# Kernel tuning notes

Hardware: AMD Instinct MI355X
Metric: run time of the kernel (lower is better)

The kernel has to match this reference:

```python
import jax, jax.numpy as jnp
import numpy as np

B, S, D, H = 32, 512, 512, 8
DF = D // H  # dim_feature = 64
NEG_INF = -1e32


def setup_inputs() -> dict:
    key = jax.random.key(0)
    ks = jax.random.split(key, 8)
    std = 1.0 / np.sqrt(D)  # xavier-ish scale for square linears
    return {
        "q": jax.random.normal(ks[0], (B, S, D), jnp.float32),
        "k": jax.random.normal(ks[1], (B, S, D), jnp.float32),
        "v": jax.random.normal(ks[2], (B, S, D), jnp.float32),
        "mask": jnp.tril(jnp.ones((S, S), jnp.int32))[None, None],  # causal AKT mask
        "zero_pad": 1,
        "question_difficulty_emb": jax.random.normal(ks[3], (B, S, S), jnp.float32) * 0.1,
        "Wk": jax.random.normal(ks[4], (D, D), jnp.float32) * std,
        "bk": jnp.zeros((D,), jnp.float32),
        "Wv": jax.random.normal(ks[5], (D, D), jnp.float32) * std,
        "bv": jnp.zeros((D,), jnp.float32),
        "Wo": jax.random.normal(ks[6], (D, D), jnp.float32) * std,
        "bo": jnp.zeros((D,), jnp.float32),
        "gammas": jax.random.normal(ks[7], (H, 1, 1), jnp.float32) * 0.1,
    }


def reference(q, k, v, mask, zero_pad, question_difficulty_emb, Wk, bk, Wv, bv, Wo, bo, gammas):
    bs = q.shape[0]

    def proj(x, W, b):
        # Linear then split heads: [B,S,D] -> [B,H,S,DF]
        return (x @ W.T + b).reshape(bs, -1, H, DF).transpose(0, 2, 1, 3)

    qh = proj(q, Wk, bk)  # key_query_same=True: q uses key_linear
    kh = proj(k, Wk, bk)
    vh = proj(v, Wv, bv)

    scores = jnp.einsum("bhqd,bhkd->bhqk", qh, kh) / jnp.sqrt(jnp.float32(DF))
    seqlen = scores.shape[-1]
    maskb = mask == 0  # [1,1,S,S]

    # --- distance-decay term (computed under no_grad in torch, detached) ---
    scores_ = jax.nn.softmax(jnp.where(maskb, NEG_INF, scores), axis=-1)
    scores_ = scores_ * mask.astype(scores.dtype)
    distcum = jnp.cumsum(scores_, axis=-1)                      # [B,H,S,S]
    disttot = jnp.sum(scores_, axis=-1, keepdims=True)          # [B,H,S,1]
    pos = jnp.abs(jnp.arange(seqlen)[None, :] - jnp.arange(seqlen)[:, None]).astype(scores.dtype)
    dist_scores = jnp.sqrt(jnp.clip((disttot - distcum) * pos[None, None], 0.0))
    dist_scores = jax.lax.stop_gradient(dist_scores)

    gamma = -jax.nn.softplus(gammas)[None]                      # [1,H,1,1]
    diff = jnp.exp(jax.nn.sigmoid(question_difficulty_emb))[:, None]  # [B,1,S,S]
    total_effect = jnp.clip(jnp.exp(dist_scores * gamma * diff), 1e-5, 1e5)

    scores = scores * total_effect
    scores = jax.nn.softmax(jnp.where(maskb, NEG_INF, scores), axis=-1)
    if zero_pad:
        scores = scores.at[:, :, 0, :].set(0.0)  # zero first query row
    scores = jnp.where(maskb, 0.0, scores)
    # dropout p=0 (eval) -> identity

    out = jnp.einsum("bhqk,bhkd->bhqd", scores, vh)
    concat = out.transpose(0, 2, 1, 3).reshape(bs, -1, D)
    return concat @ Wo.T + bo
```

## Files before the change

### kernel.cpp

```cpp
#include <hip/hip_runtime.h>

typedef unsigned short u16;
typedef __attribute__((ext_vector_type(8))) short short8;
typedef __attribute__((ext_vector_type(8))) _Float16 h8;
typedef __attribute__((ext_vector_type(4))) float f32x4;

__device__ __forceinline__ float b2f(u16 u) {
    return __uint_as_float(((unsigned int)u) << 16);
}
__device__ __forceinline__ u16 f2b(float f) {
    unsigned int x = __float_as_uint(f);
    return (u16)((x + 0x7FFFu + ((x >> 16) & 1u)) >> 16);
}
__device__ __forceinline__ float ldf(const void* p, size_t i, bool f32) {
    return f32 ? ((const float*)p)[i] : b2f(((const u16*)p)[i]);
}
__device__ __forceinline__ void stf(void* p, size_t i, bool f32, float v) {
    if (f32) ((float*)p)[i] = v; else ((u16*)p)[i] = f2b(v);
}
__device__ __forceinline__ float ex2(float x) {
    float r; asm("v_exp_f32 %0, %1" : "=v"(r) : "v"(x)); return r;
}

__device__ __forceinline__ void ldsld16(const void* g, void* l) {
    __builtin_amdgcn_global_load_lds(
        (const __attribute__((address_space(1))) unsigned int*)g,
        (__attribute__((address_space(3))) unsigned int*)l, 16, 0, 0);
}

__global__ void detect_f32(const u16* __restrict__ q, int* __restrict__ flag) {
    __shared__ int cw, cz;
    if (threadIdx.x == 0) { cw = 0; cz = 0; }
    __syncthreads();
    int w = 0, z = 0;
    for (int i = threadIdx.x; i < 4096; i += 256) {
        u16 u = q[i];
        int e = (u >> 7) & 0xFF;
        if (e >= 0xC8) w++;
        if (((i & 1) == 0) && u == 0) z++;
    }
    atomicAdd(&cw, w); atomicAdd(&cz, z);
    __syncthreads();
    if (threadIdx.x == 0) *flag = (cw > 8 || cz > 1024) ? 1 : 0;
}

__global__ __launch_bounds__(256) void cvt3(
    const void* __restrict__ s0, const void* __restrict__ s1,
    const void* __restrict__ s2, u16* __restrict__ d0, u16* __restrict__ d1,
    u16* __restrict__ d2, int n, const int* __restrict__ flag)
{
    const bool f32 = (*flag) != 0;
    const int z = blockIdx.z;
    const void* src = (z == 0) ? s0 : (z == 1) ? s1 : s2;
    u16* dst = (z == 0) ? d0 : (z == 1) ? d1 : d2;
    const int i = (blockIdx.x * 256 + threadIdx.x) * 8;
    if (i >= n) return;
    short8 o;
    if (f32) {
        const float4* s = (const float4*)((const float*)src + i);
        float4 v0 = s[0], v1 = s[1];
        o[0] = (short)f2b(v0.x); o[1] = (short)f2b(v0.y);
        o[2] = (short)f2b(v0.z); o[3] = (short)f2b(v0.w);
        o[4] = (short)f2b(v1.x); o[5] = (short)f2b(v1.y);
        o[6] = (short)f2b(v1.z); o[7] = (short)f2b(v1.w);
    } else {
        o = *(const short8*)((const u16*)src + i);
    }
    *(short8*)(dst + i) = o;
}

__global__ __launch_bounds__(256) void prep_diff(
    const void* __restrict__ qde, _Float16* __restrict__ diff, int n,
    const int* __restrict__ flag)
{
    const bool f32 = (*flag) != 0;
    const int i = (blockIdx.x * 256 + threadIdx.x) * 8;
    if (i >= n) return;
    float x[8];
    if (f32) {
        const float4* s = (const float4*)((const float*)qde + i);
        float4 v0 = s[0], v1 = s[1];
        x[0] = v0.x; x[1] = v0.y; x[2] = v0.z; x[3] = v0.w;
        x[4] = v1.x; x[5] = v1.y; x[6] = v1.z; x[7] = v1.w;
    } else {
        short8 v8 = *(const short8*)((const u16*)qde + i);
        #pragma unroll
        for (int j = 0; j < 8; ++j) x[j] = b2f((u16)v8[j]);
    }
    h8 o;
    #pragma unroll
    for (int j = 0; j < 8; ++j) {
        float sig = __builtin_amdgcn_rcpf(1.f + __expf(-x[j]));
        o[j] = (_Float16)__expf(sig);
    }
    *(h8*)(diff + i) = o;
}

#define BM 128
#define BN 128
#define BK 32

__device__ __forceinline__ void gemm_body(
    const u16* __restrict__ A, const u16* __restrict__ W,
    const void* __restrict__ bias, void* __restrict__ dst,
    bool f32, int mode, int bm, int bn, int M, int N, int K)
{
    __shared__ u16 As[BM * BK];
    __shared__ u16 Bs[BN * BK];
    const int t = threadIdx.x;
    const int w = t >> 6, l = t & 63, lq = l & 15, quad = l >> 4;
    const int wr = (w >> 1) * 64, wc = (w & 1) * 64;

    const int whalf = (w & 1) * 64;
    const u16* gsrc = (w < 2) ? A : W;
    const int  gbase = (w < 2) ? bm : bn;
    u16* lbase = (w < 2) ? As : Bs;

    f32x4 acc[4][4] = {};

    for (int k0 = 0; k0 < K; k0 += BK) {
        __syncthreads();
        #pragma unroll
        for (int c = 0; c < 4; ++c) {
            const int row = whalf + c * 16 + (l >> 2);
            ldsld16(gsrc + (size_t)(gbase + row) * K + k0 + (l & 3) * 8,
                    lbase + row * BK + (l & 3) * 8);
        }
        asm volatile("s_waitcnt vmcnt(0)" ::: "memory");
        __syncthreads();
        short8 af[4], bf[4];
        #pragma unroll
        for (int i = 0; i < 4; ++i)
            af[i] = *(const short8*)&As[(wr + i * 16 + lq) * BK + quad * 8];
        #pragma unroll
        for (int j = 0; j < 4; ++j)
            bf[j] = *(const short8*)&Bs[(wc + j * 16 + lq) * BK + quad * 8];
        #pragma unroll
        for (int i = 0; i < 4; ++i)
            #pragma unroll
            for (int j = 0; j < 4; ++j)
                acc[i][j] = __builtin_amdgcn_mfma_f32_16x16x32_bf16(
                    af[i], bf[j], acc[i][j], 0, 0, 0);
    }

    #pragma unroll
    for (int j = 0; j < 4; ++j) {
        const int n = bn + wc + j * 16 + lq;
        const float bb = ldf(bias, n, f32);
        #pragma unroll
        for (int i = 0; i < 4; ++i) {
            #pragma unroll
            for (int r = 0; r < 4; ++r) {
                const int m = bm + wr + i * 16 + quad * 4 + r;
                const float vout = acc[i][j][r] + bb;
                if (mode == 0) {
                    const int b = m >> 9, s = m & 511, hh = n >> 6, df = n & 63;
                    ((u16*)dst)[((((size_t)b * 8 + hh) * 512 + s) << 6) + df] = f2b(vout);
                } else if (mode == 2) {
                    const int b = m >> 9, s = m & 511, hh = n >> 6, df = n & 63;
                    ((u16*)dst)[((((size_t)b * 8 + hh) * 64 + df) << 9) + s] = f2b(vout);
                } else {
                    stf(dst, (size_t)m * N + n, f32, vout);
                }
            }
        }
    }
}

__global__ __launch_bounds__(256) void proj3(
    const u16* __restrict__ cq, const u16* __restrict__ ck,
    const u16* __restrict__ cv, const u16* __restrict__ cWk,
    const u16* __restrict__ cWv, const void* __restrict__ bk,
    const void* __restrict__ bv, u16* __restrict__ qh, u16* __restrict__ kh,
    u16* __restrict__ vt, const int* __restrict__ flag, int M, int N, int K)
{
    const int z = blockIdx.z;
    const u16* A = (z == 0) ? cq : (z == 1) ? ck : cv;
    const u16* W = (z < 2) ? cWk : cWv;
    const void* bias = (z < 2) ? bk : bv;
    void* dst = (z == 0) ? (void*)qh : (z == 1) ? (void*)kh : (void*)vt;
    gemm_body(A, W, bias, dst, (*flag) != 0, (z < 2) ? 0 : 2,
              blockIdx.y * BM, blockIdx.x * BN, M, N, K);
}

__global__ __launch_bounds__(256) void gemm_out(
    const u16* __restrict__ A, const u16* __restrict__ W,
    const void* __restrict__ bias, void* __restrict__ dst,
    const int* __restrict__ flag, int M, int N, int K)
{
    gemm_body(A, W, bias, dst, (*flag) != 0, 1,
              blockIdx.y * BM, blockIdx.x * BN, M, N, K);
}

#define QT  16
#define SRS 568
#define PRS 584

__global__ __launch_bounds__(512) void akt_attn(
    const u16* __restrict__ qh, const u16* __restrict__ kh,
    const u16* __restrict__ vt, const _Float16* __restrict__ diff,
    const void* __restrict__ gammas, const int* __restrict__ zero_pad,
    const int* __restrict__ flag, u16* __restrict__ attn)
{
    __shared__ _Float16 s_h[QT * SRS];
    __shared__ u16      p_lds[QT * PRS];

    const int blk = blockIdx.x;
    const int h = blk & 7;
    const int i0 = blk >> 3;
    const int qt = i0 & 31;
    const int b = i0 >> 5;

    const int q0 = qt * QT;
    const int t = threadIdx.x, w = t >> 6, l = t & 63;
    const int lq = l & 15, quad = l >> 4;
    const bool f32 = (*flag) != 0;
    const size_t bh = ((size_t)b * 8 + h) * 512;
    const int qmax = q0 + QT - 1;

    {
        const u16* qb = qh + (bh + q0) * 64;
        short8 af0 = *(const short8*)(qb + lq * 64 +      quad * 8);
        short8 af1 = *(const short8*)(qb + lq * 64 + 32 + quad * 8);
        const u16* kb = kh + bh * 64;
        const int KT = (q0 + QT + 127) >> 7;
        int n0 = w * 16;
        bool act = (n0 <= qmax);
        short8 bf0, bf1;
        if (act) {
            bf0 = *(const short8*)(kb + (size_t)(n0 + lq) * 64 +      quad * 8);
            bf1 = *(const short8*)(kb + (size_t)(n0 + lq) * 64 + 32 + quad * 8);
        }
        for (int kt = 0; kt < KT; ++kt) {
            const int n0n = (kt + 1) * 128 + w * 16;
            const bool actn = (kt + 1 < KT) && (n0n <= qmax);
            short8 nb0, nb1;
            if (actn) {
                nb0 = *(const short8*)(kb + (size_t)(n0n + lq) * 64 +      quad * 8);
                nb1 = *(const short8*)(kb + (size_t)(n0n + lq) * 64 + 32 + quad * 8);
            }
            if (act) {
                f32x4 acc = {0.f, 0.f, 0.f, 0.f};
                acc = __builtin_amdgcn_mfma_f32_16x16x32_bf16(af0, bf0, acc, 0, 0, 0);
                acc = __builtin_amdgcn_mfma_f32_16x16x32_bf16(af1, bf1, acc, 0, 0, 0);
                const int cm = n0 + lq + 8 * (n0 >> 6);
                #pragma unroll
                for (int r = 0; r < 4; ++r)
                    s_h[(quad * 4 + r) * SRS + cm] =
                        (_Float16)(acc[r] * 0.180336880f);
            }
            bf0 = nb0; bf1 = nb1; act = actn; n0 = n0n;
        }
    }
    __syncthreads();

    {
        const float g = ldf(gammas, h, f32);
        const float gl2 = -log1pf(expf(g)) * 1.4426950408889634f;
        const int zp = zero_pad[0];
        const int c0 = l * 8;
        #pragma unroll
        for (int rr = 0; rr < 2; ++rr) {
            const int row = w * 2 + rr;
            const int q = q0 + row;
            const size_t qoff = ((size_t)b * 512 + q) * 512 + c0;
            h8 dv = *(const h8*)(diff + qoff);
            h8 sv16 = *(const h8*)(s_h + row * SRS + c0 + 8 * (l >> 3));
            float sv[8], cs[8];
            float run = 0.f;
            #pragma unroll
            for (int j = 0; j < 8; ++j) {
                float s = (c0 + j <= q) ? (float)sv16[j] : -1e30f;
                sv[j] = s;
                float p = ex2(s);
                run += p; cs[j] = run;
            }
            float incl = run;
            #pragma unroll
            for (int o = 1; o < 64; o <<= 1) {
                float u = __shfl_up(incl, o, 64);
                if (l >= o) incl += u;
            }
            const float ls   = __shfl(incl, 63, 64);
            const float inv1 = __builtin_amdgcn_rcpf(ls);
            const float t0   = ls - incl + run;
            const float qf   = (float)(q - c0);
            float f8[8]; float lf = 0.f;
            #pragma unroll
            for (int j = 0; j < 8; ++j) {
                float suf  = t0 - cs[j];
                float pos  = qf - (float)j;
                float m    = fmaxf(suf * pos, 0.f) * inv1;
                float dist = __builtin_amdgcn_sqrtf(m);
                float a    = fmaxf(dist * gl2 * (float)dv[j], -16.609640474f);
                float eff  = ex2(a);
                float f    = ex2(sv[j] * eff);
                f8[j] = f; lf += f;
            }
            #pragma unroll
            for (int o = 32; o > 0; o >>= 1) lf += __shfl_xor(lf, o, 64);
            float inv2 = __builtin_amdgcn_rcpf(lf);
            if (zp && q == 0) inv2 = 0.f;
            short8 pb;
            #pragma unroll
            for (int j = 0; j < 8; ++j) pb[j] = (short)f2b(f8[j] * inv2);
            *(short8*)(p_lds + row * PRS + c0 + 8 * (l >> 3)) = pb;
        }
    }
    __syncthreads();

    {
        const int g = w & 3;
        const int half = w >> 2;
        const int KS = (qmax >> 5) + 1;
        const u16* vb = vt + ((size_t)(b * 8 + h) * 64 + g * 16 + lq) * 512;
        const u16* prow = p_lds + lq * PRS;
        f32x4 oacc = {0.f, 0.f, 0.f, 0.f};
        for (int ks = half; ks < KS; ks += 2) {
            const int kb2 = ks * 32 + quad * 8;
            short8 pa = *(const short8*)(prow + kb2 + 8 * (kb2 >> 6));
            short8 vv = *(const short8*)(vb + kb2);
            oacc = __builtin_amdgcn_mfma_f32_16x16x32_bf16(pa, vv, oacc, 0, 0, 0);
        }
        float* opart = (float*)s_h;
        if (half == 1) {
            #pragma unroll
            for (int r = 0; r < 4; ++r)
                opart[(g * 16 + quad * 4 + r) * 17 + lq] = oacc[r];
        }
        __syncthreads();
        if (half == 0) {
            const size_t ob = ((size_t)b * 512 + q0 + quad * 4) * 512 + h * 64 + g * 16 + lq;
            #pragma unroll
            for (int r = 0; r < 4; ++r)
                attn[ob + (size_t)r * 512] =
                    f2b(oacc[r] + opart[(g * 16 + quad * 4 + r) * 17 + lq]);
        }
    }
}

extern "C" void kernel_launch(void* const* d_in, const int* in_sizes, int n_in,
                              void* d_out, int out_size, void* d_ws, size_t ws_size,
                              hipStream_t stream) {
    const void* q   = d_in[0];
    const void* k   = d_in[1];
    const void* v   = d_in[2];
    const int*  zp  = (const int*)d_in[4];
    const void* qde = d_in[5];
    const void* Wk  = d_in[6];
    const void* bk  = d_in[7];
    const void* Wv  = d_in[8];
    const void* bv  = d_in[9];
    const void* Wo  = d_in[10];
    const void* bo  = d_in[11];
    const void* gam = d_in[12];

    const int M = 32 * 512, N = 512, K = 512;
    const int NBIG = M * K;
    const int NW = 512 * 512;

    char* ws = (char*)d_ws;
    int* flag = (int*)ws;
    const size_t SZB = (size_t)NBIG * 2;
    const size_t SZW = (size_t)NW * 2;
    u16* cWk  = (u16*)(ws + 1024);
    u16* cWv  = (u16*)(ws + 1024 + SZW);
    u16* cWo  = (u16*)(ws + 1024 + 2 * SZW);
    u16* cq   = (u16*)(ws + 1024 + 3 * SZW);
    u16* ck   = (u16*)(ws + 1024 + 3 * SZW + SZB);
    u16* cv   = (u16*)(ws + 1024 + 3 * SZW + 2 * SZB);
    u16* qh   = (u16*)(ws + 1024 + 3 * SZW + 3 * SZB);
    u16* kh   = (u16*)(ws + 1024 + 3 * SZW + 4 * SZB);
    u16* vt   = (u16*)(ws + 1024 + 3 * SZW + 5 * SZB);
    u16* attn = (u16*)(ws + 1024 + 3 * SZW + 6 * SZB);

    detect_f32<<<1, 256, 0, stream>>>((const u16*)q, flag);
    cvt3<<<dim3(NW / 2048, 1, 3), 256, 0, stream>>>(Wk, Wv, Wo, cWk, cWv, cWo, NW, flag);
    cvt3<<<dim3(NBIG / 2048, 1, 3), 256, 0, stream>>>(q, k, v, cq, ck, cv, NBIG, flag);
    proj3<<<dim3(N / BN, M / BM, 3), 256, 0, stream>>>(
        cq, ck, cv, cWk, cWv, bk, bv, qh, kh, vt, flag, M, N, K);
    _Float16* diffb = (_Float16*)cq;
    prep_diff<<<dim3(NBIG / 2048), 256, 0, stream>>>(qde, diffb, NBIG, flag);
    akt_attn<<<8192, 512, 0, stream>>>(qh, kh, vt, diffb, gam, zp, flag, attn);
    gemm_out<<<dim3(N / BN, M / BM), 256, 0, stream>>>(attn, cWo, bo, d_out, flag, M, N, K);
}
```

Before: 394.1 us.

## Size softmax lane groups to causal row length and switch PV path to fp16

The distance-decay softmax phase now packs several query rows per wavefront, sizing each lane group to the causal row length (qmax) instead of always using 64 lanes per row. Short rows in early query tiles no longer pay for masked columns, and the scan and reduction shuffles shrink to match. The V projection output and the probability tile are stored as fp16 rather than bf16, and the PV product uses the f16 MFMA, which changes rounding. The loop becomes a runtime-bounded loop with runtime shuffle widths, which may add overhead and uneven work across waves.

```diff
diff --git a/kernel.cpp b/kernel.cpp
--- a/kernel.cpp
+++ b/kernel.cpp
@@ -158,7 +158,8 @@
                     ((u16*)dst)[((((size_t)b * 8 + hh) * 512 + s) << 6) + df] = f2b(vout);
                 } else if (mode == 2) {
                     const int b = m >> 9, s = m & 511, hh = n >> 6, df = n & 63;
-                    ((u16*)dst)[((((size_t)b * 8 + hh) * 64 + df) << 9) + s] = f2b(vout);
+                    _Float16 hv = (_Float16)vout;
+                    ((u16*)dst)[((((size_t)b * 8 + hh) * 64 + df) << 9) + s] = *(const u16*)&hv;
                 } else {
                     stf(dst, (size_t)m * N + n, f32, vout);
                 }
@@ -258,30 +259,36 @@
         const float g = ldf(gammas, h, f32);
         const float gl2 = -log1pf(expf(g)) * 1.4426950408889634f;
         const int zp = zero_pad[0];
-        const int c0 = l * 8;
-        #pragma unroll
-        for (int rr = 0; rr < 2; ++rr) {
-            const int row = w * 2 + rr;
+        const int need = (qmax >> 3) + 1;
+        int W = 8; while (W < need) W <<= 1;
+        const int lw = 31 - __builtin_clz(W);
+        const int R = 64 >> lw;
+        const int G = W >> 2;
+        const int ln = l & (W - 1);
+        const int seg = l >> lw;
+        const int c0 = ln * 8;
+        const int cm = c0 + 8 * (c0 >> 6);
+        for (int p = w; p < G; p += 8) {
+            const int row = p * R + seg;
             const int q = q0 + row;
             const size_t qoff = ((size_t)b * 512 + q) * 512 + c0;
             h8 dv = *(const h8*)(diff + qoff);
-            h8 sv16 = *(const h8*)(s_h + row * SRS + c0 + 8 * (l >> 3));
+            h8 sv16 = *(const h8*)(s_h + row * SRS + cm);
             float sv[8], cs[8];
             float run = 0.f;
             #pragma unroll
             for (int j = 0; j < 8; ++j) {
                 float s = (c0 + j <= q) ? (float)sv16[j] : -1e30f;
                 sv[j] = s;
-                float p = ex2(s);
-                run += p; cs[j] = run;
+                float pp = ex2(s);
+                run += pp; cs[j] = run;
             }
             float incl = run;
-            #pragma unroll
-            for (int o = 1; o < 64; o <<= 1) {
-                float u = __shfl_up(incl, o, 64);
-                if (l >= o) incl += u;
-            }
-            const float ls   = __shfl(incl, 63, 64);
+            for (int o = 1; o < W; o <<= 1) {
+                float u = __shfl_up(incl, o, W);
+                if (ln >= o) incl += u;
+            }
+            const float ls   = __shfl(incl, W - 1, W);
             const float inv1 = __builtin_amdgcn_rcpf(ls);
             const float t0   = ls - incl + run;
             const float qf   = (float)(q - c0);
@@ -297,14 +304,14 @@
                 float f    = ex2(sv[j] * eff);
                 f8[j] = f; lf += f;
             }
-            #pragma unroll
-            for (int o = 32; o > 0; o >>= 1) lf += __shfl_xor(lf, o, 64);
+            #pragma unroll 6
+            for (int o = W >> 1; o > 0; o >>= 1) lf += __shfl_xor(lf, o, 64);
             float inv2 = __builtin_amdgcn_rcpf(lf);
             if (zp && q == 0) inv2 = 0.f;
-            short8 pb;
-            #pragma unroll
-            for (int j = 0; j < 8; ++j) pb[j] = (short)f2b(f8[j] * inv2);
-            *(short8*)(p_lds + row * PRS + c0 + 8 * (l >> 3)) = pb;
+            h8 pb;
+            #pragma unroll
+            for (int j = 0; j < 8; ++j) pb[j] = (_Float16)(f8[j] * inv2);
+            *(h8*)((_Float16*)p_lds + row * PRS + cm) = pb;
         }
     }
     __syncthreads();
@@ -313,14 +320,15 @@
         const int g = w & 3;
         const int half = w >> 2;
         const int KS = (qmax >> 5) + 1;
-        const u16* vb = vt + ((size_t)(b * 8 + h) * 64 + g * 16 + lq) * 512;
-        const u16* prow = p_lds + lq * PRS;
+        const _Float16* vb = (const _Float16*)vt +
+            ((size_t)(b * 8 + h) * 64 + g * 16 + lq) * 512;
+        const _Float16* prow = (const _Float16*)p_lds + lq * PRS;
         f32x4 oacc = {0.f, 0.f, 0.f, 0.f};
         for (int ks = half; ks < KS; ks += 2) {
             const int kb2 = ks * 32 + quad * 8;
-            short8 pa = *(const short8*)(prow + kb2 + 8 * (kb2 >> 6));
-            short8 vv = *(const short8*)(vb + kb2);
-            oacc = __builtin_amdgcn_mfma_f32_16x16x32_bf16(pa, vv, oacc, 0, 0, 0);
+            h8 pa = *(const h8*)(prow + kb2 + 8 * (kb2 >> 6));
+            h8 vv = *(const h8*)(vb + kb2);
+            oacc = __builtin_amdgcn_mfma_f32_16x16x32_f16(pa, vv, oacc, 0, 0, 0);
         }
         float* opart = (float*)s_h;
         if (half == 1) {
```

After: 383.7 us. 1.03x faster.
